# Kernel tuning notes

Measured on AMD Instinct MI355X. Metric: run time of the kernel, lower is better.

The kernel has to match this reference:

```python
import jax, jax.numpy as jnp
import numpy as np

NUM_AGENTS = 8
D_AGENT = 64  # input_dim_single_agent
INPUT_DIM = NUM_AGENTS * D_AGENT
NORM_TERM = NUM_AGENTS - 1 if NUM_AGENTS > 1 else 1
BATCH = 65536


def setup_inputs() -> dict:
    key = jax.random.key(0)
    k1, k2, k3 = jax.random.split(key, 3)
    x = jax.random.normal(k1, (BATCH, INPUT_DIM), dtype=jnp.float32)
    # original code multiplies hidden_weights by 0.1 (twice-written bug leaves comm unscaled)
    hidden_weights = jax.random.normal(k2, (D_AGENT, D_AGENT), dtype=jnp.float32) * 0.1
    communication_weights = jax.random.normal(k3, (D_AGENT, D_AGENT), dtype=jnp.float32)
    return {"x": x, "hidden_weights": hidden_weights,
            "communication_weights": communication_weights}


def reference(x, hidden_weights, communication_weights):
    # Equivalent to y = tanh(x @ final_mat.T) where final_mat has diagonal
    # [d,d] blocks = hidden_weights and off-diagonal blocks = comm/(A-1).
    B = x.shape[0]
    xb = x.reshape(B, NUM_AGENTS, D_AGENT)          # [B, A, d]
    others = xb.sum(axis=1, keepdims=True) - xb      # sum over other agents
    # F.linear uses weight W with out = x @ W.T, hence 'ed' contraction on d
    y = (jnp.einsum('bad,ed->bae', xb, hidden_weights)
         + jnp.einsum('bad,ed->bae', others, communication_weights) / NORM_TERM)
    return jnp.tanh(y).reshape(B, INPUT_DIM)
```

## Files before the change

### kernel.cpp

```cpp
#include <hip/hip_runtime.h>


typedef _Float16 half4v  __attribute__((ext_vector_type(4)));
typedef _Float16 half8v  __attribute__((ext_vector_type(8)));
typedef float    floatx4 __attribute__((ext_vector_type(4)));

#define WAVES_PER_BLOCK 4
#define BSTRIDE 144

__device__ __forceinline__ half8v h8_bfly_add(half8v v, int mask) {
    union { half8v h; int i[4]; } u, r;
    u.h = v;
    #pragma unroll
    for (int k = 0; k < 4; ++k) r.i[k] = __shfl_xor(u.i[k], mask, 64);
    return v + r.h;
}

__global__ __launch_bounds__(256, 8)
void comm_kernel(const float* __restrict__ x,
                 const float* __restrict__ Hw,
                 const float* __restrict__ Cw,
                 float* __restrict__ out)
{
    __shared__ __align__(16) _Float16 augB[64 * BSTRIDE];

    const int tid  = threadIdx.x;
    const int lane = tid & 63;
    const int wave = tid >> 6;
    const int quad = lane >> 4;
    const int l16  = lane & 15;

    #pragma unroll
    for (int i = 0; i < 4; ++i) {
        const int idx = i * 256 + tid;
        const int e = idx >> 4;
        const int k = (idx & 15) << 2;
        const float4 h = *reinterpret_cast<const float4*>(Hw + e * 64 + k);
        const float4 c = *reinterpret_cast<const float4*>(Cw + e * 64 + k);
        half4v m4, c4;
        m4[0] = (_Float16)(h.x - c.x * (1.0f / 7.0f)); c4[0] = (_Float16)(c.x * (1.0f / 7.0f));
        m4[1] = (_Float16)(h.y - c.y * (1.0f / 7.0f)); c4[1] = (_Float16)(c.y * (1.0f / 7.0f));
        m4[2] = (_Float16)(h.z - c.z * (1.0f / 7.0f)); c4[2] = (_Float16)(c.z * (1.0f / 7.0f));
        m4[3] = (_Float16)(h.w - c.w * (1.0f / 7.0f)); c4[3] = (_Float16)(c.w * (1.0f / 7.0f));
        *reinterpret_cast<half4v*>(&augB[e * BSTRIDE + k])      = m4;
        *reinterpret_cast<half4v*>(&augB[e * BSTRIDE + 64 + k]) = c4;
    }
    __syncthreads();

    const int wgid = blockIdx.x * WAVES_PER_BLOCK + wave;
    const float* xi = x + (size_t)wgid * 1024 + l16 * 64 + quad * 8;
    float* o = out + (size_t)wgid * 1024 + l16 * 64 + quad * 4;

    const float4 v0 = *reinterpret_cast<const float4*>(xi);
    const float4 v1 = *reinterpret_cast<const float4*>(xi + 4);
    const float4 v2 = *reinterpret_cast<const float4*>(xi + 32);
    const float4 v3 = *reinterpret_cast<const float4*>(xi + 36);

    half8v a0, a1;
    a0[0]=(_Float16)v0.x; a0[1]=(_Float16)v0.y; a0[2]=(_Float16)v0.z; a0[3]=(_Float16)v0.w;
    a0[4]=(_Float16)v1.x; a0[5]=(_Float16)v1.y; a0[6]=(_Float16)v1.z; a0[7]=(_Float16)v1.w;
    a1[0]=(_Float16)v2.x; a1[1]=(_Float16)v2.y; a1[2]=(_Float16)v2.z; a1[3]=(_Float16)v2.w;
    a1[4]=(_Float16)v3.x; a1[5]=(_Float16)v3.y; a1[6]=(_Float16)v3.z; a1[7]=(_Float16)v3.w;

    half8v s0 = a0, s1 = a1;
    #pragma unroll
    for (int m = 1; m <= 4; m <<= 1) {
        s0 = h8_bfly_add(s0, m);
        s1 = h8_bfly_add(s1, m);
    }

    floatx4 acc[4];
    #pragma unroll
    for (int nt = 0; nt < 4; ++nt) acc[nt] = floatx4{0.f, 0.f, 0.f, 0.f};

    #pragma unroll
    for (int nt = 0; nt < 4; ++nt) {
        const _Float16* bp = &augB[(nt * 16 + l16) * BSTRIDE + quad * 8];
        const half8v b0 = *reinterpret_cast<const half8v*>(bp);
        const half8v b1 = *reinterpret_cast<const half8v*>(bp + 32);
        const half8v b2 = *reinterpret_cast<const half8v*>(bp + 64);
        const half8v b3 = *reinterpret_cast<const half8v*>(bp + 96);
        acc[nt] = __builtin_amdgcn_mfma_f32_16x16x32_f16(b0, a0, acc[nt], 0, 0, 0);
        acc[nt] = __builtin_amdgcn_mfma_f32_16x16x32_f16(b1, a1, acc[nt], 0, 0, 0);
        acc[nt] = __builtin_amdgcn_mfma_f32_16x16x32_f16(b2, s0, acc[nt], 0, 0, 0);
        acc[nt] = __builtin_amdgcn_mfma_f32_16x16x32_f16(b3, s1, acc[nt], 0, 0, 0);
    }

    #pragma unroll
    for (int nt = 0; nt < 4; ++nt) {
        floatx4 r;
        #pragma unroll
        for (int reg = 0; reg < 4; ++reg) {
            float y = acc[nt][reg];
            y = fminf(10.f, fmaxf(-10.f, y));
            const float tv  = __builtin_amdgcn_exp2f(y * 2.8853900817779268f);
            r[reg] = (tv - 1.f) * __builtin_amdgcn_rcpf(tv + 1.f);
        }
        *reinterpret_cast<floatx4*>(o + nt * 16) = r;
    }
}

extern "C" void kernel_launch(void* const* d_in, const int* in_sizes, int n_in,
                              void* d_out, int out_size, void* d_ws, size_t ws_size,
                              hipStream_t stream) {
    const float* x  = (const float*)d_in[0];
    const float* Hw = (const float*)d_in[1];
    const float* Cw = (const float*)d_in[2];
    float* out = (float*)d_out;

    const int rows   = in_sizes[0] / 512;
    const int ntiles = rows * 8 / 16;
    const int blocks = ntiles / WAVES_PER_BLOCK;
    comm_kernel<<<blocks, 256, 0, stream>>>(x, Hw, Cw, out);
}
```

Before: 228.2 us.

## Load weight fragments directly from global memory instead of LDS staging

```diff
diff --git a/kernel.cpp b/kernel.cpp
--- a/kernel.cpp
+++ b/kernel.cpp
@@ -1,12 +1,10 @@
 #include <hip/hip_runtime.h>
 
 
-typedef _Float16 half4v  __attribute__((ext_vector_type(4)));
 typedef _Float16 half8v  __attribute__((ext_vector_type(8)));
 typedef float    floatx4 __attribute__((ext_vector_type(4)));
 
 #define WAVES_PER_BLOCK 4
-#define BSTRIDE 144
 
 __device__ __forceinline__ half8v h8_bfly_add(half8v v, int mask) {
     union { half8v h; int i[4]; } u, r;
@@ -16,36 +14,33 @@
     return v + r.h;
 }
 
-__global__ __launch_bounds__(256, 8)
+__device__ __forceinline__ void cvt_mc(const float4 h0, const float4 h1,
+                                       const float4 c0, const float4 c1,
+                                       half8v& m, half8v& cn) {
+    const float r7 = 1.0f / 7.0f;
+    const float n0 = c0.x * r7, n1 = c0.y * r7, n2 = c0.z * r7, n3 = c0.w * r7;
+    const float n4 = c1.x * r7, n5 = c1.y * r7, n6 = c1.z * r7, n7 = c1.w * r7;
+    m[0] = (_Float16)(h0.x - n0); m[1] = (_Float16)(h0.y - n1);
+    m[2] = (_Float16)(h0.z - n2); m[3] = (_Float16)(h0.w - n3);
+    m[4] = (_Float16)(h1.x - n4); m[5] = (_Float16)(h1.y - n5);
+    m[6] = (_Float16)(h1.z - n6); m[7] = (_Float16)(h1.w - n7);
+    cn[0] = (_Float16)n0; cn[1] = (_Float16)n1;
+    cn[2] = (_Float16)n2; cn[3] = (_Float16)n3;
+    cn[4] = (_Float16)n4; cn[5] = (_Float16)n5;
+    cn[6] = (_Float16)n6; cn[7] = (_Float16)n7;
+}
+
+__global__ __launch_bounds__(256, 4)
 void comm_kernel(const float* __restrict__ x,
                  const float* __restrict__ Hw,
                  const float* __restrict__ Cw,
                  float* __restrict__ out)
 {
-    __shared__ __align__(16) _Float16 augB[64 * BSTRIDE];
-
     const int tid  = threadIdx.x;
     const int lane = tid & 63;
     const int wave = tid >> 6;
     const int quad = lane >> 4;
     const int l16  = lane & 15;
-
-    #pragma unroll
-    for (int i = 0; i < 4; ++i) {
-        const int idx = i * 256 + tid;
-        const int e = idx >> 4;
-        const int k = (idx & 15) << 2;
-        const float4 h = *reinterpret_cast<const float4*>(Hw + e * 64 + k);
-        const float4 c = *reinterpret_cast<const float4*>(Cw + e * 64 + k);
-        half4v m4, c4;
-        m4[0] = (_Float16)(h.x - c.x * (1.0f / 7.0f)); c4[0] = (_Float16)(c.x * (1.0f / 7.0f));
-        m4[1] = (_Float16)(h.y - c.y * (1.0f / 7.0f)); c4[1] = (_Float16)(c.y * (1.0f / 7.0f));
-        m4[2] = (_Float16)(h.z - c.z * (1.0f / 7.0f)); c4[2] = (_Float16)(c.z * (1.0f / 7.0f));
-        m4[3] = (_Float16)(h.w - c.w * (1.0f / 7.0f)); c4[3] = (_Float16)(c.w * (1.0f / 7.0f));
-        *reinterpret_cast<half4v*>(&augB[e * BSTRIDE + k])      = m4;
-        *reinterpret_cast<half4v*>(&augB[e * BSTRIDE + 64 + k]) = c4;
-    }
-    __syncthreads();
 
     const int wgid = blockIdx.x * WAVES_PER_BLOCK + wave;
     const float* xi = x + (size_t)wgid * 1024 + l16 * 64 + quad * 8;
@@ -75,11 +70,22 @@
 
     #pragma unroll
     for (int nt = 0; nt < 4; ++nt) {
-        const _Float16* bp = &augB[(nt * 16 + l16) * BSTRIDE + quad * 8];
-        const half8v b0 = *reinterpret_cast<const half8v*>(bp);
-        const half8v b1 = *reinterpret_cast<const half8v*>(bp + 32);
-        const half8v b2 = *reinterpret_cast<const half8v*>(bp + 64);
-        const half8v b3 = *reinterpret_cast<const half8v*>(bp + 96);
+        const int e = nt * 16 + l16;
+        const float* Hp = Hw + e * 64 + quad * 8;
+        const float* Cp = Cw + e * 64 + quad * 8;
+        const float4 h00 = *reinterpret_cast<const float4*>(Hp);
+        const float4 h01 = *reinterpret_cast<const float4*>(Hp + 4);
+        const float4 h10 = *reinterpret_cast<const float4*>(Hp + 32);
+        const float4 h11 = *reinterpret_cast<const float4*>(Hp + 36);
+        const float4 c00 = *reinterpret_cast<const float4*>(Cp);
+        const float4 c01 = *reinterpret_cast<const float4*>(Cp + 4);
+        const float4 c10 = *reinterpret_cast<const float4*>(Cp + 32);
+        const float4 c11 = *reinterpret_cast<const float4*>(Cp + 36);
+
+        half8v b0, b1, b2, b3;
+        cvt_mc(h00, h01, c00, c01, b0, b2);
+        cvt_mc(h10, h11, c10, c11, b1, b3);
+
         acc[nt] = __builtin_amdgcn_mfma_f32_16x16x32_f16(b0, a0, acc[nt], 0, 0, 0);
         acc[nt] = __builtin_amdgcn_mfma_f32_16x16x32_f16(b1, a1, acc[nt], 0, 0, 0);
         acc[nt] = __builtin_amdgcn_mfma_f32_16x16x32_f16(b2, s0, acc[nt], 0, 0, 0);
```

Measured after the change: 304.1 us. 1.33x slower.
